# Performance work log

Hardware: AMD Instinct MI355X
Metric: run time of the kernel (lower is better)

## Reference

```python
import jax, jax.numpy as jnp
import numpy as np

PH, PW = 8, 8
HEADS = 8
EPS = 1e-6
N_ITER = 1
SHIFTS = [(dh, dw) for dh in (-1, 0, 1) for dw in (-1, 0, 1)]  # row-major 3x3, matches eye(9) kernels


def unfold3(x):
    # x: (B, C, H, W) -> (B, C, 9, H, W); out[..., i, h, w] = x[..., h+dh_i, w+dw_i] (zero pad)
    B, C, H, W = x.shape
    xp = jnp.pad(x, ((0, 0), (0, 0), (1, 1), (1, 1)))
    return jnp.stack([xp[:, :, 1 + dh:1 + dh + H, 1 + dw:1 + dw + W] for dh, dw in SHIFTS], axis=2)


def fold3(y):
    # y: (..., 9, H, W) -> (..., H, W); transpose of unfold3 (scatter-add of the 9 shifted planes)
    H, W = y.shape[-2], y.shape[-1]
    pad = [(0, 0)] * (y.ndim - 2) + [(1, 1), (1, 1)]
    yp = jnp.pad(y, pad)
    out = jnp.zeros(y.shape[:-3] + (H, W), y.dtype)
    for i, (dh, dw) in enumerate(SHIFTS):
        out = out + yp[..., i, 1 - dh:1 - dh + H, 1 - dw:1 - dw + W]
    return out


def layernorm_cf(x, w, b):
    # channels_first LayerNorm over dim=1
    mu = x.mean(1, keepdims=True)
    var = ((x - mu) ** 2).mean(1, keepdims=True)
    return w[None, :, None, None] * (x - mu) / jnp.sqrt(var + EPS) + b[None, :, None, None]


def mha_bchw(x, qkv_w, proj_w, proj_b):
    B, C, H, W = x.shape
    hd = C // HEADS
    t = x.reshape(B, C, H * W).transpose(0, 2, 1)  # (B, N, C)
    qkv = (t @ qkv_w.T).reshape(B, H * W, 3, HEADS, hd).transpose(2, 0, 3, 1, 4)
    q, k, v = qkv[0], qkv[1], qkv[2]  # (B, h, N, hd)
    attn = jax.nn.softmax(jnp.einsum('bhnd,bhmd->bhnm', q, k) * (hd ** -0.5), axis=-1)
    o = jnp.einsum('bhnm,bhmd->bhnd', attn, v).transpose(0, 2, 1, 3).reshape(B, H * W, C)
    o = o @ proj_w.T + proj_b
    return o.transpose(0, 2, 1).reshape(B, C, H, W)


def reference(x, ln_w, ln_b, qkv_w, proj_w, proj_b):
    x = layernorm_cf(x, ln_w, ln_b)
    B, C, H, W = x.shape
    Hs, Ws = H // PH, W // PW
    N = Hs * Ws
    scale = C ** -0.5
    # adaptive avg pool == block mean (H, W divisible by PH, PW)
    xb = x.reshape(B, C, Hs, PH, Ws, PW)
    stoken = xb.mean(axis=(3, 5))                                # (B, C, Hs, Ws)
    pix = xb.transpose(0, 2, 4, 3, 5, 1).reshape(B, N, PH * PW, C)  # (B, N, pp, C)

    def unfold_tok(sf):
        u = unfold3(sf)  # (B, C, 9, Hs, Ws)
        return u.transpose(0, 3, 4, 1, 2).reshape(B, N, C, 9)

    sf = stoken
    aff = None
    aff_sum = None
    for idx in range(N_ITER):  # torch.no_grad() loop
        st = unfold_tok(sf)
        aff = jax.nn.softmax(jnp.einsum('bnpc,bnck->bnpk', pix, st) * scale, axis=-1)  # (B, N, pp, 9)
        aff_sum = fold3(aff.sum(2).transpose(0, 2, 1).reshape(B, 9, Hs, Ws))[:, None]  # (B, 1, Hs, Ws)
        if idx < N_ITER - 1:
            sf = jnp.einsum('bnpc,bnpk->bnck', pix, aff).transpose(0, 2, 3, 1).reshape(B, C, 9, Hs, Ws)
            sf = fold3(sf) / (aff_sum + 1e-12)
    aff = jax.lax.stop_gradient(aff)
    aff_sum = jax.lax.stop_gradient(aff_sum)

    sf = jnp.einsum('bnpc,bnpk->bnck', pix, aff).transpose(0, 2, 3, 1).reshape(B, C, 9, Hs, Ws)
    sf = fold3(sf) / (aff_sum + 1e-12)                            # (B, C, Hs, Ws)
    sf = mha_bchw(sf, qkv_w, proj_w, proj_b)                      # refine
    st = unfold_tok(sf)                                           # (B, N, C, 9)
    out = jnp.einsum('bnck,bnpk->bncp', st, aff)                  # (B, N, C, pp)
    out = out.reshape(B, Hs, Ws, C, PH, PW).transpose(0, 3, 1, 4, 2, 5).reshape(B, C, H, W)
    return out


def setup_inputs() -> dict:
    key = jax.random.key(0)
    k1, k2, k3 = jax.random.split(key, 3)
    C = 128
    return {
        'x': jax.random.normal(k1, (8, C, 256, 256), dtype=jnp.float32),
        'ln_w': jnp.ones((C,), jnp.float32),
        'ln_b': jnp.zeros((C,), jnp.float32),
        'qkv_w': jax.random.normal(k2, (3 * C, C), dtype=jnp.float32) * 0.02,
        'proj_w': jax.random.normal(k3, (C, C), dtype=jnp.float32) * 0.02,
        'proj_b': jnp.zeros((C,), jnp.float32),
    }
```

## Files before the change

kernel.cpp:

```cpp
#include <hip/hip_runtime.h>
#include <cstdint>
#include <cstddef>

#define B_    8
#define C_    128
#define H_    256
#define W_    256
#define HWSZ  (256*256)
#define HS_   32
#define WS_   32
#define NTOK  1024
#define PP_   64
#define EPS_  1e-6f
#define SCALE_QK 0.08838834764831845f
#define SCALE_AT 0.25f

__device__ __forceinline__ int swz8(int wg, int chunk) {
  return (wg & 7) * chunk + (wg >> 3);
}

__global__ __launch_bounds__(256) void k1_ln_stoken(
    const float* __restrict__ x, const float* __restrict__ lnw, const float* __restrict__ lnb,
    float* __restrict__ stok, float* __restrict__ gmu, float* __restrict__ grs)
{
  __shared__ __align__(16) float sp[64*128];
  __shared__ float reds[4*64], redq[4*64];
  __shared__ float smu[64], srs[64];
  int wg = swz8(blockIdx.x, 1024);
  int b = wg >> 10, n = wg & 1023;
  int hs = n >> 5, ws = n & 31;
  int tid = threadIdx.x;

  int p = tid & 63;
  int pi = p >> 3, pj = p & 7;
  const float* xpix = x + (size_t)b*C_*HWSZ + (size_t)(hs*8 + pi)*W_ + (ws*8 + pj);
  #pragma unroll
  for (int it = 0; it < 8; ++it) {
    int cb = it*4 + (tid >> 6);
    int c0 = cb*4;
    float v0 = xpix[(size_t)(c0+0)*HWSZ];
    float v1 = xpix[(size_t)(c0+1)*HWSZ];
    float v2 = xpix[(size_t)(c0+2)*HWSZ];
    float v3 = xpix[(size_t)(c0+3)*HWSZ];
    float4 v; v.x=v0; v.y=v1; v.z=v2; v.w=v3;
    *(float4*)&sp[p*128 + 4*(cb ^ (p & 7))] = v;
  }
  __syncthreads();
  {
    int pp2 = tid & 63, cq = tid >> 6;
    float s = 0.f, q = 0.f;
    #pragma unroll
    for (int e = 0; e < 8; ++e) {
      int cb = cq*8 + e;
      float4 v = *(const float4*)&sp[pp2*128 + 4*(cb ^ (pp2 & 7))];
      s += v.x + v.y + v.z + v.w;
      q += v.x*v.x + v.y*v.y + v.z*v.z + v.w*v.w;
    }
    reds[cq*64 + pp2] = s; redq[cq*64 + pp2] = q;
  }
  __syncthreads();
  if (tid < 64) {
    float s = reds[tid] + reds[64+tid] + reds[128+tid] + reds[192+tid];
    float q = redq[tid] + redq[64+tid] + redq[128+tid] + redq[192+tid];
    float mu = s * (1.f/128.f);
    float var = q * (1.f/128.f) - mu*mu;
    float rs = rsqrtf(var + EPS_);
    smu[tid] = mu; srs[tid] = rs;
    size_t base = (size_t)wg*64 + tid;
    gmu[base] = mu; grs[base] = rs;
  }
  __syncthreads();
  {
    int c = tid >> 1, ph = tid & 1;
    float s = 0.f;
    #pragma unroll
    for (int q = 0; q < 32; ++q) {
      int pr = ph*32 + q;
      float v = sp[pr*128 + 4*((c >> 2) ^ (pr & 7)) + (c & 3)];
      s += (v - smu[pr]) * srs[pr];
    }
    s += __shfl_xor(s, 1);
    if (ph == 0)
      stok[(size_t)wg*128 + c] = lnw[c] * (s * (1.f/64.f)) + lnb[c];
  }
}

__global__ __launch_bounds__(256) void k2_aff(
    const float* __restrict__ x, const float* __restrict__ lnw, const float* __restrict__ lnb,
    const float* __restrict__ stok, const float* __restrict__ gmu, const float* __restrict__ grs,
    float* __restrict__ aff_g, float* __restrict__ affsum, float* __restrict__ sf0)
{
  __shared__ __align__(16) float sp[64*128];
  __shared__ __align__(16) float st_s[9*128];
  __shared__ __align__(16) float aff_s[64*12];
  __shared__ float smu[64], srs[64], wl[128], bl[128];
  __shared__ float red[4*16*36];
  int wg = swz8(blockIdx.x, 1024);
  int b = wg >> 10, n = wg & 1023, hs = n >> 5, ws = n & 31;
  int tid = threadIdx.x;

  if (tid < 64) { smu[tid] = gmu[(size_t)wg*64 + tid]; srs[tid] = grs[(size_t)wg*64 + tid]; }
  else if (tid < 192) { int l = tid - 64; wl[l] = lnw[l]; bl[l] = lnb[l]; }
  for (int l = tid; l < 1152; l += 256) {
    int k = l >> 7, c = l & 127;
    int dh = k/3 - 1, dw = k - (k/3)*3 - 1;
    int hs2 = hs + dh, ws2 = ws + dw;
    float v = 0.f;
    if ((unsigned)hs2 < 32u && (unsigned)ws2 < 32u)
      v = stok[((size_t)b*NTOK + hs2*32 + ws2)*128 + c];
    st_s[l] = v;
  }
  __syncthreads();
  {
    int p = tid & 63;
    int pi = p >> 3, pj = p & 7;
    const float* xpix = x + (size_t)b*C_*HWSZ + (size_t)(hs*8 + pi)*W_ + (ws*8 + pj);
    float mu = smu[p], rs = srs[p];
    #pragma unroll
    for (int it = 0; it < 8; ++it) {
      int cb = it*4 + (tid >> 6);
      int c0 = cb*4;
      float v0 = xpix[(size_t)(c0+0)*HWSZ];
      float v1 = xpix[(size_t)(c0+1)*HWSZ];
      float v2 = xpix[(size_t)(c0+2)*HWSZ];
      float v3 = xpix[(size_t)(c0+3)*HWSZ];
      float4 y;
      y.x = wl[c0+0]*((v0-mu)*rs) + bl[c0+0];
      y.y = wl[c0+1]*((v1-mu)*rs) + bl[c0+1];
      y.z = wl[c0+2]*((v2-mu)*rs) + bl[c0+2];
      y.w = wl[c0+3]*((v3-mu)*rs) + bl[c0+3];
      *(float4*)&sp[p*128 + 4*(cb ^ (p & 7))] = y;
    }
  }
  __syncthreads();
  {
    int pg = tid & 15;
    int cg = tid >> 4;
    float pr[4][8];
    #pragma unroll
    for (int r = 0; r < 4; ++r) {
      int p2 = 4*pg + r;
      #pragma unroll
      for (int hh = 0; hh < 2; ++hh) {
        int cb = 2*cg + hh;
        float4 v = *(const float4*)&sp[p2*128 + 4*(cb ^ (p2 & 7))];
        pr[r][hh*4+0]=v.x; pr[r][hh*4+1]=v.y; pr[r][hh*4+2]=v.z; pr[r][hh*4+3]=v.w;
      }
    }
    float acc[4][9];
    #pragma unroll
    for (int r = 0; r < 4; ++r)
      #pragma unroll
      for (int k = 0; k < 9; ++k) acc[r][k] = 0.f;
    #pragma unroll
    for (int k = 0; k < 9; ++k) {
      float4 s0 = *(const float4*)&st_s[k*128 + 8*cg];
      float4 s1 = *(const float4*)&st_s[k*128 + 8*cg + 4];
      #pragma unroll
      for (int r = 0; r < 4; ++r)
        acc[r][k] += pr[r][0]*s0.x + pr[r][1]*s0.y + pr[r][2]*s0.z + pr[r][3]*s0.w
                   + pr[r][4]*s1.x + pr[r][5]*s1.y + pr[r][6]*s1.z + pr[r][7]*s1.w;
    }
    #pragma unroll
    for (int r = 0; r < 4; ++r)
      #pragma unroll
      for (int k = 0; k < 9; ++k) {
        float v = acc[r][k];
        v += __shfl_xor(v, 16);
        v += __shfl_xor(v, 32);
        acc[r][k] = v;
      }
    if ((tid & 48) == 0) {
      int w = tid >> 6;
      #pragma unroll
      for (int r = 0; r < 4; ++r)
        #pragma unroll
        for (int k = 0; k < 9; ++k)
          red[(w*16 + pg)*36 + r*9 + k] = acc[r][k];
    }
  }
  __syncthreads();
  for (int l = tid; l < 576; l += 256) {
    float v = red[l] + red[576+l] + red[1152+l] + red[1728+l];
    int pg = l/36, rem = l - pg*36;
    int r = rem/9, k = rem - r*9;
    aff_s[(4*pg + r)*12 + k] = v * SCALE_QK;
  }
  __syncthreads();
  if (tid < 64) {
    float mx = -1e30f;
    #pragma unroll
    for (int k = 0; k < 9; ++k) mx = fmaxf(mx, aff_s[tid*12 + k]);
    float e[9]; float ssum = 0.f;
    #pragma unroll
    for (int k = 0; k < 9; ++k) { e[k] = __expf(aff_s[tid*12 + k] - mx); ssum += e[k]; }
    float inv = 1.f / ssum;
    #pragma unroll
    for (int k = 0; k < 9; ++k) aff_s[tid*12 + k] = e[k]*inv;
  }
  __syncthreads();
  for (int l = tid; l < 576; l += 256) {
    int p2 = l/9, k = l - p2*9;
    aff_g[(size_t)wg*576 + l] = aff_s[p2*12 + k];
  }
  if (tid < 9) {
    int k = tid;
    float s = 0.f;
    for (int p2 = 0; p2 < 64; ++p2) s += aff_s[p2*12 + k];
    int dh = k/3 - 1, dw = k - (k/3)*3 - 1;
    int hs2 = hs + dh, ws2 = ws + dw;
    if ((unsigned)hs2 < 32u && (unsigned)ws2 < 32u)
      atomicAdd(&affsum[(size_t)b*NTOK + hs2*32 + ws2], s);
  }
  float a2[4][9];
  {
    int cq = tid & 31;
    int pg3 = tid >> 5;
    #pragma unroll
    for (int e = 0; e < 4; ++e)
      #pragma unroll
      for (int k = 0; k < 9; ++k) a2[e][k] = 0.f;
    #pragma unroll
    for (int pp = 0; pp < 8; ++pp) {
      int p2 = 8*pg3 + pp;
      float4 pv = *(const float4*)&sp[p2*128 + 4*(cq ^ (p2 & 7))];
      float4 a0 = *(const float4*)&aff_s[p2*12];
      float4 a1 = *(const float4*)&aff_s[p2*12 + 4];
      float a8 = aff_s[p2*12 + 8];
      float av[9] = {a0.x,a0.y,a0.z,a0.w,a1.x,a1.y,a1.z,a1.w,a8};
      #pragma unroll
      for (int k = 0; k < 9; ++k) {
        float a = av[k];
        a2[0][k] += pv.x*a; a2[1][k] += pv.y*a; a2[2][k] += pv.z*a; a2[3][k] += pv.w*a;
      }
    }
    #pragma unroll
    for (int e = 0; e < 4; ++e)
      #pragma unroll
      for (int k = 0; k < 9; ++k)
        a2[e][k] += __shfl_xor(a2[e][k], 32);
  }
  __syncthreads();
  float* red2 = sp;
  {
    int cq = tid & 31, w = tid >> 6;
    if ((tid & 32) == 0) {
      #pragma unroll
      for (int e = 0; e < 4; ++e)
        #pragma unroll
        for (int k = 0; k < 9; ++k)
          red2[(w*32 + cq)*36 + e*9 + k] = a2[e][k];
    }
  }
  __syncthreads();
  for (int l = tid; l < 1152; l += 256) {
    float v = red2[l] + red2[1152+l] + red2[2304+l] + red2[3456+l];
    int cq = l/36, rem = l - cq*36;
    int e = rem/9, k = rem - e*9;
    int c = 4*cq + e;
    int dh = k/3 - 1, dw = k - (k/3)*3 - 1;
    int hs2 = hs + dh, ws2 = ws + dw;
    if ((unsigned)hs2 < 32u && (unsigned)ws2 < 32u)
      atomicAdd(&sf0[((size_t)b*NTOK + hs2*32 + ws2)*128 + c], v);
  }
}

__global__ __launch_bounds__(256) void k4_qkv(
    const float* __restrict__ sf0, const float* __restrict__ affsum,
    const float* __restrict__ qw, float* __restrict__ qkv)
{
  __shared__ __align__(16) float As[64*132];
  __shared__ float Bs[64*129];
  __shared__ float rs_s[64];
  int m0 = blockIdx.x*64, j0 = blockIdx.y*64;
  int tid = threadIdx.x;
  if (tid < 64) rs_s[tid] = 1.f / (affsum[m0 + tid] + 1e-12f);
  __syncthreads();
  for (int l = tid; l < 2048; l += 256) {
    int m = l >> 5, kq = l & 31;
    float4 v = *(const float4*)&sf0[(size_t)(m0+m)*128 + 4*kq];
    float rd = rs_s[m];
    v.x*=rd; v.y*=rd; v.z*=rd; v.w*=rd;
    *(float4*)&As[m*132 + 4*kq] = v;
  }
  for (int l = tid; l < 2048; l += 256) {
    int j = l >> 5, kq = l & 31;
    float4 v = *(const float4*)&qw[(size_t)(j0+j)*128 + 4*kq];
    Bs[j*129 + 4*kq+0]=v.x; Bs[j*129 + 4*kq+1]=v.y; Bs[j*129 + 4*kq+2]=v.z; Bs[j*129 + 4*kq+3]=v.w;
  }
  __syncthreads();
  int tj = tid & 15, tm = tid >> 4;
  float acc[4][4];
  #pragma unroll
  for (int r = 0; r < 4; ++r)
    #pragma unroll
    for (int s = 0; s < 4; ++s) acc[r][s] = 0.f;
  for (int kk = 0; kk < 128; ++kk) {
    float a0 = As[(4*tm+0)*132+kk], a1 = As[(4*tm+1)*132+kk], a2v = As[(4*tm+2)*132+kk], a3 = As[(4*tm+3)*132+kk];
    float b0 = Bs[(4*tj+0)*129+kk], b1 = Bs[(4*tj+1)*129+kk], b2 = Bs[(4*tj+2)*129+kk], b3 = Bs[(4*tj+3)*129+kk];
    acc[0][0]+=a0*b0; acc[0][1]+=a0*b1; acc[0][2]+=a0*b2; acc[0][3]+=a0*b3;
    acc[1][0]+=a1*b0; acc[1][1]+=a1*b1; acc[1][2]+=a1*b2; acc[1][3]+=a1*b3;
    acc[2][0]+=a2v*b0; acc[2][1]+=a2v*b1; acc[2][2]+=a2v*b2; acc[2][3]+=a2v*b3;
    acc[3][0]+=a3*b0; acc[3][1]+=a3*b1; acc[3][2]+=a3*b2; acc[3][3]+=a3*b3;
  }
  #pragma unroll
  for (int r = 0; r < 4; ++r) {
    float4 v; v.x=acc[r][0]; v.y=acc[r][1]; v.z=acc[r][2]; v.w=acc[r][3];
    *(float4*)&qkv[(size_t)(m0 + 4*tm + r)*384 + j0 + 4*tj] = v;
  }
}

__global__ __launch_bounds__(128) void k5_attn(const float* __restrict__ qkv, float* __restrict__ o2)
{
  int wg = swz8(blockIdx.x, 64);
  int bh = wg >> 3, qt = wg & 7;
  int b = bh >> 3, h = bh & 7;
  int tid = threadIdx.x;
  size_t tok = (size_t)b*NTOK + qt*128 + tid;
  const float* qp = qkv + tok*384 + h*16;
  float q[16];
  #pragma unroll
  for (int e = 0; e < 4; ++e) {
    float4 v = *(const float4*)&qp[4*e];
    q[4*e]=v.x; q[4*e+1]=v.y; q[4*e+2]=v.z; q[4*e+3]=v.w;
  }
  const float* kb = qkv + (size_t)b*NTOK*384 + 128 + h*16;
  const float* vb = kb + 128;
  float m = -1e30f, l = 0.f, o[16];
  #pragma unroll
  for (int e = 0; e < 16; ++e) o[e] = 0.f;
  for (int ch = 0; ch < 64; ++ch) {
    float s[16];
    #pragma unroll
    for (int jj = 0; jj < 16; ++jj) {
      const float* kr = kb + (size_t)(ch*16 + jj)*384;
      float d = 0.f;
      #pragma unroll
      for (int e = 0; e < 4; ++e) {
        float4 kv = *(const float4*)&kr[4*e];
        d += q[4*e]*kv.x + q[4*e+1]*kv.y + q[4*e+2]*kv.z + q[4*e+3]*kv.w;
      }
      s[jj] = d * SCALE_AT;
    }
    float cm = s[0];
    #pragma unroll
    for (int jj = 1; jj < 16; ++jj) cm = fmaxf(cm, s[jj]);
    float mn = fmaxf(m, cm);
    float corr = __expf(m - mn);
    l *= corr;
    #pragma unroll
    for (int e = 0; e < 16; ++e) o[e] *= corr;
    #pragma unroll
    for (int jj = 0; jj < 16; ++jj) {
      float e1 = __expf(s[jj] - mn);
      l += e1;
      const float* vr = vb + (size_t)(ch*16 + jj)*384;
      #pragma unroll
      for (int e = 0; e < 4; ++e) {
        float4 vv = *(const float4*)&vr[4*e];
        o[4*e]+=e1*vv.x; o[4*e+1]+=e1*vv.y; o[4*e+2]+=e1*vv.z; o[4*e+3]+=e1*vv.w;
      }
    }
    m = mn;
  }
  float inv = 1.f / l;
  float* op = o2 + tok*128 + h*16;
  #pragma unroll
  for (int e = 0; e < 4; ++e) {
    float4 v; v.x=o[4*e]*inv; v.y=o[4*e+1]*inv; v.z=o[4*e+2]*inv; v.w=o[4*e+3]*inv;
    *(float4*)&op[4*e] = v;
  }
}

__global__ __launch_bounds__(256) void k6_proj(
    const float* __restrict__ o2, const float* __restrict__ pw,
    const float* __restrict__ pb, float* __restrict__ sfn)
{
  __shared__ __align__(16) float As[64*132];
  __shared__ float Bs[64*129];
  int m0 = blockIdx.x*64, j0 = blockIdx.y*64;
  int tid = threadIdx.x;
  for (int l = tid; l < 2048; l += 256) {
    int m = l >> 5, kq = l & 31;
    float4 v = *(const float4*)&o2[(size_t)(m0+m)*128 + 4*kq];
    *(float4*)&As[m*132 + 4*kq] = v;
  }
  for (int l = tid; l < 2048; l += 256) {
    int j = l >> 5, kq = l & 31;
    float4 v = *(const float4*)&pw[(size_t)(j0+j)*128 + 4*kq];
    Bs[j*129 + 4*kq+0]=v.x; Bs[j*129 + 4*kq+1]=v.y; Bs[j*129 + 4*kq+2]=v.z; Bs[j*129 + 4*kq+3]=v.w;
  }
  __syncthreads();
  int tj = tid & 15, tm = tid >> 4;
  float acc[4][4];
  #pragma unroll
  for (int r = 0; r < 4; ++r)
    #pragma unroll
    for (int s = 0; s < 4; ++s) acc[r][s] = 0.f;
  for (int kk = 0; kk < 128; ++kk) {
    float a0 = As[(4*tm+0)*132+kk], a1 = As[(4*tm+1)*132+kk], a2v = As[(4*tm+2)*132+kk], a3 = As[(4*tm+3)*132+kk];
    float b0 = Bs[(4*tj+0)*129+kk], b1 = Bs[(4*tj+1)*129+kk], b2 = Bs[(4*tj+2)*129+kk], b3 = Bs[(4*tj+3)*129+kk];
    acc[0][0]+=a0*b0; acc[0][1]+=a0*b1; acc[0][2]+=a0*b2; acc[0][3]+=a0*b3;
    acc[1][0]+=a1*b0; acc[1][1]+=a1*b1; acc[1][2]+=a1*b2; acc[1][3]+=a1*b3;
    acc[2][0]+=a2v*b0; acc[2][1]+=a2v*b1; acc[2][2]+=a2v*b2; acc[2][3]+=a2v*b3;
    acc[3][0]+=a3*b0; acc[3][1]+=a3*b1; acc[3][2]+=a3*b2; acc[3][3]+=a3*b3;
  }
  float bx = pb[j0+4*tj+0], by = pb[j0+4*tj+1], bz = pb[j0+4*tj+2], bw = pb[j0+4*tj+3];
  #pragma unroll
  for (int r = 0; r < 4; ++r) {
    float4 v; v.x=acc[r][0]+bx; v.y=acc[r][1]+by; v.z=acc[r][2]+bz; v.w=acc[r][3]+bw;
    *(float4*)&sfn[(size_t)(m0 + 4*tm + r)*128 + j0 + 4*tj] = v;
  }
}

__global__ __launch_bounds__(256) void k7_out(
    const float* __restrict__ sfn, const float* __restrict__ aff_g, float* __restrict__ out)
{
  __shared__ __align__(16) float st2[9*128];
  __shared__ __align__(16) float aff_s[64*12];
  int wg = swz8(blockIdx.x, 1024);
  int b = wg >> 10, n = wg & 1023, hs = n >> 5, ws = n & 31;
  int tid = threadIdx.x;
  for (int l = tid; l < 1152; l += 256) {
    int k = l >> 7, c = l & 127;
    int dh = k/3 - 1, dw = k - (k/3)*3 - 1;
    int hs2 = hs + dh, ws2 = ws + dw;
    float v = 0.f;
    if ((unsigned)hs2 < 32u && (unsigned)ws2 < 32u)
      v = sfn[((size_t)b*NTOK + hs2*32 + ws2)*128 + c];
    st2[l] = v;
  }
  for (int l = tid; l < 576; l += 256) {
    int p = l/9, k = l - p*9;
    aff_s[p*12 + k] = aff_g[(size_t)wg*576 + l];
  }
  __syncthreads();
  int cq = tid & 31;
  int pg = tid >> 5;
  float sr[9][4];
  #pragma unroll
  for (int k = 0; k < 9; ++k) {
    float4 v = *(const float4*)&st2[k*128 + 4*cq];
    sr[k][0]=v.x; sr[k][1]=v.y; sr[k][2]=v.z; sr[k][3]=v.w;
  }
  float ob[4][8];
  #pragma unroll
  for (int pp = 0; pp < 8; ++pp) {
    int p = 8*pg + pp;
    float4 a0 = *(const float4*)&aff_s[p*12];
    float4 a1 = *(const float4*)&aff_s[p*12 + 4];
    float a8 = aff_s[p*12 + 8];
    float av[9] = {a0.x,a0.y,a0.z,a0.w,a1.x,a1.y,a1.z,a1.w,a8};
    #pragma unroll
    for (int e = 0; e < 4; ++e) {
      float acc = 0.f;
      #pragma unroll
      for (int k = 0; k < 9; ++k) acc += sr[k][e]*av[k];
      ob[e][pp] = acc;
    }
  }
  #pragma unroll
  for (int e = 0; e < 4; ++e) {
    int c = 4*cq + e;
    float* dst = out + (((size_t)b*C_ + c)*H_ + (hs*8 + pg))*W_ + ws*8;
    float4 v0; v0.x=ob[e][0]; v0.y=ob[e][1]; v0.z=ob[e][2]; v0.w=ob[e][3];
    float4 v1; v1.x=ob[e][4]; v1.y=ob[e][5]; v1.z=ob[e][6]; v1.w=ob[e][7];
    *(float4*)&dst[0] = v0;
    *(float4*)&dst[4] = v1;
  }
}

extern "C" void kernel_launch(void* const* d_in, const int* in_sizes, int n_in,
                              void* d_out, int out_size, void* d_ws, size_t ws_size,
                              hipStream_t stream) {
  const float* x    = (const float*)d_in[0];
  const float* lnw  = (const float*)d_in[1];
  const float* lnb  = (const float*)d_in[2];
  const float* qkvw = (const float*)d_in[3];
  const float* projw= (const float*)d_in[4];
  const float* projb= (const float*)d_in[5];
  float* out = (float*)d_out;

  float* ws   = (float*)d_ws;
  float* stok = ws;
  float* gmu  = stok + 1048576;
  float* grs  = gmu  + 524288;
  float* aff  = grs  + 524288;
  float* afs  = aff  + 4718592;
  float* sf0  = afs  + 8192;
  float* qkv  = sf0  + 1048576;
  float* o2   = qkv  + 3145728;
  float* sfn  = o2   + 1048576;

  hipMemsetAsync(sf0, 0, (size_t)1048576*4, stream);
  hipMemsetAsync(afs, 0, (size_t)8192*4, stream);

  k1_ln_stoken<<<dim3(8192), dim3(256), 0, stream>>>(x, lnw, lnb, stok, gmu, grs);
  k2_aff<<<dim3(8192), dim3(256), 0, stream>>>(x, lnw, lnb, stok, gmu, grs, aff, afs, sf0);
  k4_qkv<<<dim3(128, 6), dim3(256), 0, stream>>>(sf0, afs, qkvw, qkv);
  k5_attn<<<dim3(512), dim3(128), 0, stream>>>(qkv, o2);
  k6_proj<<<dim3(128, 2), dim3(256), 0, stream>>>(o2, projw, projb, sfn);
  k7_out<<<dim3(8192), dim3(256), 0, stream>>>(sfn, aff, out);
}
```

Baseline: 1.212 ms.

## Split attention KV across lanes and swizzle GEMM shared memory for float4 reads

The attention kernel now splits each query's key/value range across 8 lanes, using 2048 blocks of 256 threads instead of 512 blocks of 128. Each lane runs its own online softmax, and the partial states are merged with xor shuffles. This raises parallelism and occupancy for a kernel that previously had only 64K threads each scanning all 1024 keys. The qkv and proj GEMMs replace padded shared-memory layouts with an XOR-swizzled layout so loads and stores can use float4, at the cost of more shuffle and exp work in the merge.

```diff
diff --git a/kernel.cpp b/kernel.cpp
--- a/kernel.cpp
+++ b/kernel.cpp
@@ -269,8 +269,8 @@
     const float* __restrict__ sf0, const float* __restrict__ affsum,
     const float* __restrict__ qw, float* __restrict__ qkv)
 {
-  __shared__ __align__(16) float As[64*132];
-  __shared__ float Bs[64*129];
+  __shared__ __align__(16) float As[64*128];
+  __shared__ __align__(16) float Bs[64*128];
   __shared__ float rs_s[64];
   int m0 = blockIdx.x*64, j0 = blockIdx.y*64;
   int tid = threadIdx.x;
@@ -281,12 +281,12 @@
     float4 v = *(const float4*)&sf0[(size_t)(m0+m)*128 + 4*kq];
     float rd = rs_s[m];
     v.x*=rd; v.y*=rd; v.z*=rd; v.w*=rd;
-    *(float4*)&As[m*132 + 4*kq] = v;
+    *(float4*)&As[m*128 + 4*(kq ^ ((m>>2) & 7))] = v;
   }
   for (int l = tid; l < 2048; l += 256) {
     int j = l >> 5, kq = l & 31;
     float4 v = *(const float4*)&qw[(size_t)(j0+j)*128 + 4*kq];
-    Bs[j*129 + 4*kq+0]=v.x; Bs[j*129 + 4*kq+1]=v.y; Bs[j*129 + 4*kq+2]=v.z; Bs[j*129 + 4*kq+3]=v.w;
+    *(float4*)&Bs[j*128 + 4*(kq ^ ((j>>2) & 7))] = v;
   }
   __syncthreads();
   int tj = tid & 15, tm = tid >> 4;
@@ -295,13 +295,19 @@
   for (int r = 0; r < 4; ++r)
     #pragma unroll
     for (int s = 0; s < 4; ++s) acc[r][s] = 0.f;
-  for (int kk = 0; kk < 128; ++kk) {
-    float a0 = As[(4*tm+0)*132+kk], a1 = As[(4*tm+1)*132+kk], a2v = As[(4*tm+2)*132+kk], a3 = As[(4*tm+3)*132+kk];
-    float b0 = Bs[(4*tj+0)*129+kk], b1 = Bs[(4*tj+1)*129+kk], b2 = Bs[(4*tj+2)*129+kk], b3 = Bs[(4*tj+3)*129+kk];
-    acc[0][0]+=a0*b0; acc[0][1]+=a0*b1; acc[0][2]+=a0*b2; acc[0][3]+=a0*b3;
-    acc[1][0]+=a1*b0; acc[1][1]+=a1*b1; acc[1][2]+=a1*b2; acc[1][3]+=a1*b3;
-    acc[2][0]+=a2v*b0; acc[2][1]+=a2v*b1; acc[2][2]+=a2v*b2; acc[2][3]+=a2v*b3;
-    acc[3][0]+=a3*b0; acc[3][1]+=a3*b1; acc[3][2]+=a3*b2; acc[3][3]+=a3*b3;
+  for (int kq = 0; kq < 32; ++kq) {
+    float4 a[4], bq[4];
+    #pragma unroll
+    for (int r = 0; r < 4; ++r)
+      a[r] = *(const float4*)&As[(4*tm+r)*128 + 4*(kq ^ (tm & 7))];
+    #pragma unroll
+    for (int s = 0; s < 4; ++s)
+      bq[s] = *(const float4*)&Bs[(4*tj+s)*128 + 4*(kq ^ (tj & 7))];
+    #pragma unroll
+    for (int r = 0; r < 4; ++r)
+      #pragma unroll
+      for (int s = 0; s < 4; ++s)
+        acc[r][s] += a[r].x*bq[s].x + a[r].y*bq[s].y + a[r].z*bq[s].z + a[r].w*bq[s].w;
   }
   #pragma unroll
   for (int r = 0; r < 4; ++r) {
@@ -310,14 +316,18 @@
   }
 }
 
-__global__ __launch_bounds__(128) void k5_attn(const float* __restrict__ qkv, float* __restrict__ o2)
+__global__ __launch_bounds__(256) void k5_attn(const float* __restrict__ qkv, float* __restrict__ o2)
 {
-  int wg = swz8(blockIdx.x, 64);
-  int bh = wg >> 3, qt = wg & 7;
+  int wg = swz8(blockIdx.x, 256);
+  int bh = wg >> 5;
+  int tt = wg & 31;
   int b = bh >> 3, h = bh & 7;
   int tid = threadIdx.x;
-  size_t tok = (size_t)b*NTOK + qt*128 + tid;
-  const float* qp = qkv + tok*384 + h*16;
+  int wave = tid >> 6, lane = tid & 63;
+  int ql = lane & 7, sp = lane >> 3;
+  int t = tt*32 + wave*8 + ql;
+
+  const float* qp = qkv + ((size_t)b*NTOK + t)*384 + h*16;
   float q[16];
   #pragma unroll
   for (int e = 0; e < 4; ++e) {
@@ -329,46 +339,67 @@
   float m = -1e30f, l = 0.f, o[16];
   #pragma unroll
   for (int e = 0; e < 16; ++e) o[e] = 0.f;
-  for (int ch = 0; ch < 64; ++ch) {
-    float s[16];
-    #pragma unroll
-    for (int jj = 0; jj < 16; ++jj) {
-      const float* kr = kb + (size_t)(ch*16 + jj)*384;
+
+  for (int c = 0; c < 16; ++c) {
+    float s[8];
+    #pragma unroll
+    for (int j = 0; j < 8; ++j) {
+      int kv = (c*8 + j)*8 + sp;
+      const float* kr = kb + (size_t)kv*384;
       float d = 0.f;
       #pragma unroll
       for (int e = 0; e < 4; ++e) {
-        float4 kv = *(const float4*)&kr[4*e];
-        d += q[4*e]*kv.x + q[4*e+1]*kv.y + q[4*e+2]*kv.z + q[4*e+3]*kv.w;
+        float4 kvv = *(const float4*)&kr[4*e];
+        d += q[4*e]*kvv.x + q[4*e+1]*kvv.y + q[4*e+2]*kvv.z + q[4*e+3]*kvv.w;
       }
-      s[jj] = d * SCALE_AT;
+      s[j] = d * SCALE_AT;
     }
     float cm = s[0];
     #pragma unroll
-    for (int jj = 1; jj < 16; ++jj) cm = fmaxf(cm, s[jj]);
+    for (int j = 1; j < 8; ++j) cm = fmaxf(cm, s[j]);
     float mn = fmaxf(m, cm);
     float corr = __expf(m - mn);
     l *= corr;
     #pragma unroll
     for (int e = 0; e < 16; ++e) o[e] *= corr;
     #pragma unroll
-    for (int jj = 0; jj < 16; ++jj) {
-      float e1 = __expf(s[jj] - mn);
+    for (int j = 0; j < 8; ++j) {
+      float e1 = __expf(s[j] - mn);
       l += e1;
-      const float* vr = vb + (size_t)(ch*16 + jj)*384;
+      int kv = (c*8 + j)*8 + sp;
+      const float* vr = vb + (size_t)kv*384;
       #pragma unroll
       for (int e = 0; e < 4; ++e) {
         float4 vv = *(const float4*)&vr[4*e];
-        o[4*e]+=e1*vv.x; o[4*e+1]+=e1*vv.y; o[4*e+2]+=e1*vv.z; o[4*e+3]+=e1*vv.w;
+        o[4*e]   += e1*vv.x; o[4*e+1] += e1*vv.y;
+        o[4*e+2] += e1*vv.z; o[4*e+3] += e1*vv.w;
       }
     }
     m = mn;
   }
-  float inv = 1.f / l;
-  float* op = o2 + tok*128 + h*16;
-  #pragma unroll
-  for (int e = 0; e < 4; ++e) {
-    float4 v; v.x=o[4*e]*inv; v.y=o[4*e+1]*inv; v.z=o[4*e+2]*inv; v.w=o[4*e+3]*inv;
-    *(float4*)&op[4*e] = v;
+
+  #pragma unroll
+  for (int d = 8; d <= 32; d <<= 1) {
+    float mo = __shfl_xor(m, d);
+    float lo = __shfl_xor(l, d);
+    float M  = fmaxf(m, mo);
+    float ca = __expf(m - M), cb = __expf(mo - M);
+    #pragma unroll
+    for (int e = 0; e < 16; ++e) {
+      float oo = __shfl_xor(o[e], d);
+      o[e] = o[e]*ca + oo*cb;
+    }
+    l = l*ca + lo*cb;
+    m = M;
+  }
+  if (sp == 0) {
+    float inv = 1.f / l;
+    float* op = o2 + ((size_t)b*NTOK + t)*128 + h*16;
+    #pragma unroll
+    for (int e = 0; e < 4; ++e) {
+      float4 v; v.x=o[4*e]*inv; v.y=o[4*e+1]*inv; v.z=o[4*e+2]*inv; v.w=o[4*e+3]*inv;
+      *(float4*)&op[4*e] = v;
+    }
   }
 }
 
@@ -376,19 +407,19 @@
     const float* __restrict__ o2, const float* __restrict__ pw,
     const float* __restrict__ pb, float* __restrict__ sfn)
 {
-  __shared__ __align__(16) float As[64*132];
-  __shared__ float Bs[64*129];
+  __shared__ __align__(16) float As[64*128];
+  __shared__ __align__(16) float Bs[64*128];
   int m0 = blockIdx.x*64, j0 = blockIdx.y*64;
   int tid = threadIdx.x;
   for (int l = tid; l < 2048; l += 256) {
     int m = l >> 5, kq = l & 31;
     float4 v = *(const float4*)&o2[(size_t)(m0+m)*128 + 4*kq];
-    *(float4*)&As[m*132 + 4*kq] = v;
+    *(float4*)&As[m*128 + 4*(kq ^ ((m>>2) & 7))] = v;
   }
   for (int l = tid; l < 2048; l += 256) {
     int j = l >> 5, kq = l & 31;
     float4 v = *(const float4*)&pw[(size_t)(j0+j)*128 + 4*kq];
-    Bs[j*129 + 4*kq+0]=v.x; Bs[j*129 + 4*kq+1]=v.y; Bs[j*129 + 4*kq+2]=v.z; Bs[j*129 + 4*kq+3]=v.w;
+    *(float4*)&Bs[j*128 + 4*(kq ^ ((j>>2) & 7))] = v;
   }
   __syncthreads();
   int tj = tid & 15, tm = tid >> 4;
@@ -397,13 +428,19 @@
   for (int r = 0; r < 4; ++r)
     #pragma unroll
     for (int s = 0; s < 4; ++s) acc[r][s] = 0.f;
-  for (int kk = 0; kk < 128; ++kk) {
-    float a0 = As[(4*tm+0)*132+kk], a1 = As[(4*tm+1)*132+kk], a2v = As[(4*tm+2)*132+kk], a3 = As[(4*tm+3)*132+kk];
-    float b0 = Bs[(4*tj+0)*129+kk], b1 = Bs[(4*tj+1)*129+kk], b2 = Bs[(4*tj+2)*129+kk], b3 = Bs[(4*tj+3)*129+kk];
-    acc[0][0]+=a0*b0; acc[0][1]+=a0*b1; acc[0][2]+=a0*b2; acc[0][3]+=a0*b3;
-    acc[1][0]+=a1*b0; acc[1][1]+=a1*b1; acc[1][2]+=a1*b2; acc[1][3]+=a1*b3;
-    acc[2][0]+=a2v*b0; acc[2][1]+=a2v*b1; acc[2][2]+=a2v*b2; acc[2][3]+=a2v*b3;
-    acc[3][0]+=a3*b0; acc[3][1]+=a3*b1; acc[3][2]+=a3*b2; acc[3][3]+=a3*b3;
+  for (int kq = 0; kq < 32; ++kq) {
+    float4 a[4], bq[4];
+    #pragma unroll
+    for (int r = 0; r < 4; ++r)
+      a[r] = *(const float4*)&As[(4*tm+r)*128 + 4*(kq ^ (tm & 7))];
+    #pragma unroll
+    for (int s = 0; s < 4; ++s)
+      bq[s] = *(const float4*)&Bs[(4*tj+s)*128 + 4*(kq ^ (tj & 7))];
+    #pragma unroll
+    for (int r = 0; r < 4; ++r)
+      #pragma unroll
+      for (int s = 0; s < 4; ++s)
+        acc[r][s] += a[r].x*bq[s].x + a[r].y*bq[s].y + a[r].z*bq[s].z + a[r].w*bq[s].w;
   }
   float bx = pb[j0+4*tj+0], by = pb[j0+4*tj+1], bz = pb[j0+4*tj+2], bw = pb[j0+4*tj+3];
   #pragma unroll
@@ -498,7 +535,7 @@
   k1_ln_stoken<<<dim3(8192), dim3(256), 0, stream>>>(x, lnw, lnb, stok, gmu, grs);
   k2_aff<<<dim3(8192), dim3(256), 0, stream>>>(x, lnw, lnb, stok, gmu, grs, aff, afs, sf0);
   k4_qkv<<<dim3(128, 6), dim3(256), 0, stream>>>(sf0, afs, qkvw, qkv);
-  k5_attn<<<dim3(512), dim3(128), 0, stream>>>(qkv, o2);
+  k5_attn<<<dim3(2048), dim3(256), 0, stream>>>(qkv, o2);
   k6_proj<<<dim3(128, 2), dim3(256), 0, stream>>>(o2, projw, projb, sfn);
   k7_out<<<dim3(8192), dim3(256), 0, stream>>>(sfn, aff, out);
 }
```

Measured after the change: 975.1 us. 19.5% less time.
